# Optimization experiments

Hardware: AMD Instinct MI355X
Metric: run time of the kernel (lower is better)

Reference implementation:

```python
import jax, jax.numpy as jnp
import numpy as np

SHAPES = ((100, 100), (50, 50), (25, 25))  # (H_l, W_l) per level
D, HEADS, HD, L, P = 256, 8, 32, 3, 4


def setup_inputs() -> dict:
    key = jax.random.key(0)
    ks = jax.random.split(key, 12)
    B = 2
    Nq = sum(h * w for h, w in SHAPES)  # 13125
    inp = {
        "query": jax.random.normal(ks[0], (B, Nq, D), jnp.float32),
        "reference_points": jax.random.uniform(ks[1], (B, Nq, L, 2), jnp.float32),
        "value0": jax.random.normal(ks[2], (B, SHAPES[0][0] * SHAPES[0][1], D), jnp.float32),
        "value1": jax.random.normal(ks[3], (B, SHAPES[1][0] * SHAPES[1][1], D), jnp.float32),
        "value2": jax.random.normal(ks[4], (B, SHAPES[2][0] * SHAPES[2][1], D), jnp.float32),
        "W_val": jax.random.normal(ks[5], (D, D), jnp.float32) * 0.05,
        "b_val": jnp.zeros((D,), jnp.float32),
        "W_off": jax.random.normal(ks[6], (D, HEADS * L * P * 2), jnp.float32) * 0.01,
        "b_off": jax.random.normal(ks[7], (HEADS * L * P * 2,), jnp.float32) * 2.0,
        "W_attn": jax.random.normal(ks[8], (D, HEADS * L * P), jnp.float32) * 0.02,
        "b_attn": jnp.zeros((HEADS * L * P,), jnp.float32),
        "W_out": jax.random.normal(ks[9], (D, D), jnp.float32) * 0.05,
        "b_out": jnp.zeros((D,), jnp.float32),
    }
    return inp


def _bilinear_sample(v, Hl, Wl, loc):
    """v: (B, heads, Hl*Wl, hd); loc: (B, Nq, heads, P, 2) normalized coords in [0,1].
    Matches torch F.grid_sample(mode='bilinear', padding_mode='zeros', align_corners=False)
    applied to grid = 2*loc - 1. Returns (B, Nq, heads, P, hd)."""
    B, heads, _, hd = v.shape
    Nq, Pn = loc.shape[1], loc.shape[3]
    # align_corners=False: pixel = ((g+1)*size - 1)/2 with g = 2*loc-1  ->  loc*size - 0.5
    x = loc[..., 0] * Wl - 0.5
    y = loc[..., 1] * Hl - 0.5
    x0 = jnp.floor(x)
    y0 = jnp.floor(y)
    wx1 = x - x0
    wy1 = y - y0
    out = jnp.zeros((B, Nq, heads, Pn, hd), v.dtype)
    for xi, wx in ((x0, 1.0 - wx1), (x0 + 1.0, wx1)):
        for yi, wy in ((y0, 1.0 - wy1), (y0 + 1.0, wy1)):
            inb = (xi >= 0) & (xi < Wl) & (yi >= 0) & (yi < Hl)
            idx = (jnp.clip(yi, 0, Hl - 1) * Wl + jnp.clip(xi, 0, Wl - 1)).astype(jnp.int32)
            idx_t = idx.transpose(0, 2, 1, 3).reshape(B, heads, Nq * Pn)  # (B,H,Nq*P)
            g = jnp.take_along_axis(v, idx_t[..., None], axis=2)  # (B,H,Nq*P,hd)
            g = g.reshape(B, heads, Nq, Pn, hd).transpose(0, 2, 1, 3, 4)
            w = (wx * wy * inb).astype(v.dtype)  # (B,Nq,heads,P)
            out = out + g * w[..., None]
    return out


def _forward(query, reference_points, values, W_val, b_val, W_off, b_off, W_attn, b_attn, W_out, b_out):
    B, Nq, _ = query.shape
    offs = (query @ W_off + b_off).reshape(B, Nq, HEADS, L, P, 2)
    attn = jax.nn.softmax((query @ W_attn + b_attn).reshape(B, Nq, HEADS, L * P), axis=-1)
    attn = attn.reshape(B, Nq, HEADS, L, P)
    out = jnp.zeros((B, Nq, HEADS, HD), query.dtype)
    for lvl, (Hl, Wl) in enumerate(SHAPES):
        # project values, split heads: (B, heads, H*W, hd)
        v = (values[lvl] @ W_val + b_val).reshape(B, Hl * Wl, HEADS, HD).transpose(0, 2, 1, 3)
        norm = jnp.array([Wl, Hl], query.dtype)
        loc = reference_points[:, :, lvl][:, :, None, None, :] + offs[:, :, :, lvl] / norm  # (B,Nq,heads,P,2)
        sampled = _bilinear_sample(v, Hl, Wl, loc)  # (B,Nq,heads,P,hd)
        out = out + jnp.einsum('bnhp,bnhpd->bnhd', attn[:, :, :, lvl], sampled)
    out = out.reshape(B, Nq, D)
    return out @ W_out + b_out  # dropout is identity at eval


def reference(query, reference_points, value0, value1, value2, W_val, b_val, W_off, b_off, W_attn, b_attn, W_out, b_out):
    return _forward(query, reference_points, (value0, value1, value2), W_val, b_val, W_off, b_off, W_attn, b_attn, W_out, b_out)
```

## Files before the change

### kernel.cpp

```cpp
#include <hip/hip_runtime.h>
#include <hip/hip_bf16.h>
#include <math.h>

#define BATCH 2
#define NQ    13125
#define MQ    26250
#define DM    256
#define NH    8
#define HDIM  32
#define NL    3
#define NP    4
#define NTOK  13125
#define HSTRIDE (MQ * 32)

typedef __attribute__((ext_vector_type(8))) short bf16x8;
typedef __attribute__((ext_vector_type(4))) float f32x4;
typedef __attribute__((ext_vector_type(2))) float f32x2;

__device__ __forceinline__ short f2bf(float f) {
    unsigned u = __float_as_uint(f);
    unsigned r = (u + 0x7FFFu + ((u >> 16) & 1u)) >> 16;
    return (short)r;
}
__device__ __forceinline__ float bf2f(unsigned short u) {
    return __uint_as_float((unsigned)u << 16);
}
__device__ __forceinline__ unsigned cvt_pk_bf16(float lo, float hi) {
    unsigned r;
    asm("v_cvt_pk_bf16_f32 %0, %1, %2" : "=v"(r) : "v"(lo), "v"(hi));
    return r;
}

__device__ __forceinline__ void gld_lds16(const short* g, short* l) {
    __builtin_amdgcn_global_load_lds(
        (const __attribute__((address_space(1))) unsigned int*)g,
        (__attribute__((address_space(3))) unsigned int*)l, 16, 0, 0);
}

__global__ __launch_bounds__(256) void wprep_kernel(const float* __restrict__ Wv,
                                                    const float* __restrict__ Wo,
                                                    const float* __restrict__ Wa,
                                                    const float* __restrict__ Wu,
                                                    short* __restrict__ Wt)
{
    const int bid = blockIdx.x;
    const int w  = bid >> 8;
    const int Ns[5]   = {256, 192, 96, 256, 96};
    const int Offs[5] = {0, 65536, 114688, 163840, 139264};
    const int N = Ns[w];
    const int flat = (bid & 255) * 256 + threadIdx.x;
    const int n = flat >> 8, k = flat & 255;
    if (n >= N) return;
    if (w == 4) { Wt[139264 + n * 256 + k] = 0; return; }
    const float* W = (w == 0) ? Wv : ((w == 1) ? Wo : ((w == 2) ? Wa : Wu));
    Wt[Offs[w] + n * 256 + k] = f2bf(W[k * N + n]);
}

__global__ __launch_bounds__(512) void gemm5_kernel(const float* __restrict__ query,
                                                    const float* __restrict__ v0,
                                                    const float* __restrict__ v1,
                                                    const float* __restrict__ v2,
                                                    const short* __restrict__ Wt_val,
                                                    const short* __restrict__ Wt_off,
                                                    const float* __restrict__ b_val,
                                                    const float* __restrict__ b_off,
                                                    const float* __restrict__ b_attn,
                                                    short* __restrict__ vws,
                                                    float* __restrict__ offs,
                                                    float* __restrict__ lgts)
{
    const int e = (blockIdx.x & 7) * 129 + (blockIdx.x >> 3);
    if (e >= 1030) return;
    const int y  = e % 5;
    const int m0 = (e / 5) * 128;

    __shared__ short As[2][128 * 32];
    __shared__ short Bs[2][128 * 32];

    const int tid  = threadIdx.x;
    const bool isv = (y < 2);
    const short* Wt = isv ? Wt_val : Wt_off;
    const int n0 = isv ? y * 128 : (y - 2) * 128;

    const int r  = tid >> 2;
    const int qh = tid & 3;
    const int gm = m0 + r;
    const int gmc = (gm < MQ) ? gm : (MQ - 1);
    const float* Arow;
    if (isv) {
        const int b  = gmc / NTOK;
        const int rr = gmc % NTOK;
        if (rr < 10000)      Arow = v0 + (size_t)(b * 10000 + rr) * 256;
        else if (rr < 12500) Arow = v1 + (size_t)(b * 2500 + rr - 10000) * 256;
        else                 Arow = v2 + (size_t)(b * 625 + rr - 12500) * 256;
    } else {
        Arow = query + (size_t)gmc * 256;
    }
    const int pA = (qh ^ ((r >> 1) & 3)) << 3;

    const int kqs = qh ^ ((r >> 1) & 3);
    const short* gB = Wt + (size_t)(n0 + r) * 256 + kqs * 8;
    short* lB[2] = { Bs[0] + tid * 8, Bs[1] + tid * 8 };

    const int lane = tid & 63;
    const int wave = tid >> 6;
    const int wm   = (wave & 1) * 64;
    const int wn   = (wave >> 1) * 32;
    const int ml   = lane & 15;
    const int kq   = lane >> 4;

    f32x4 acc[4][2] = {};

    {
        gld_lds16(gB, lB[0]);
        const float4 a0 = *(const float4*)(Arow + qh * 8 + 0);
        const float4 a1 = *(const float4*)(Arow + qh * 8 + 4);
        union { bf16x8 v; unsigned u[4]; } t0;
        t0.u[0] = cvt_pk_bf16(a0.x, a0.y); t0.u[1] = cvt_pk_bf16(a0.z, a0.w);
        t0.u[2] = cvt_pk_bf16(a1.x, a1.y); t0.u[3] = cvt_pk_bf16(a1.z, a1.w);
        *(bf16x8*)(As[0] + r * 32 + pA) = t0.v;
    }
    __syncthreads();

#pragma unroll
    for (int t = 0; t < 8; ++t) {
        const int cur = t & 1, nxt = cur ^ 1;
        const int k0  = t * 32;

        float4 a0, a1;
        if (t < 7) {
            gld_lds16(gB + k0 + 32, lB[nxt]);
            a0 = *(const float4*)(Arow + k0 + 32 + qh * 8 + 0);
            a1 = *(const float4*)(Arow + k0 + 32 + qh * 8 + 4);
        }

        bf16x8 af[4], bfr[2];
#pragma unroll
        for (int ti = 0; ti < 4; ++ti) {
            const int rr = wm + ti * 16 + ml;
            af[ti] = *(const bf16x8*)&As[cur][rr * 32 + ((kq ^ ((rr >> 1) & 3)) << 3)];
        }
#pragma unroll
        for (int tj = 0; tj < 2; ++tj) {
            const int rr = wn + tj * 16 + ml;
            bfr[tj] = *(const bf16x8*)&Bs[cur][rr * 32 + ((kq ^ ((rr >> 1) & 3)) << 3)];
        }
#pragma unroll
        for (int ti = 0; ti < 4; ++ti)
#pragma unroll
            for (int tj = 0; tj < 2; ++tj)
                acc[ti][tj] = __builtin_amdgcn_mfma_f32_16x16x32_bf16(af[ti], bfr[tj], acc[ti][tj], 0, 0, 0);

        if (t < 7) {
            union { bf16x8 v; unsigned u[4]; } t0;
            t0.u[0] = cvt_pk_bf16(a0.x, a0.y); t0.u[1] = cvt_pk_bf16(a0.z, a0.w);
            t0.u[2] = cvt_pk_bf16(a1.x, a1.y); t0.u[3] = cvt_pk_bf16(a1.z, a1.w);
            *(bf16x8*)(As[nxt] + r * 32 + pA) = t0.v;
        }
        __syncthreads();
    }

#pragma unroll
    for (int tj = 0; tj < 2; ++tj) {
        const int gn = n0 + wn + tj * 16 + ml;
#pragma unroll
        for (int ti = 0; ti < 4; ++ti) {
#pragma unroll
            for (int rr = 0; rr < 4; ++rr) {
                const int gmo = m0 + wm + ti * 16 + kq * 4 + rr;
                if (gmo >= MQ) continue;
                const float v = acc[ti][tj][rr];
                if (isv) {
                    vws[(size_t)(gn >> 5) * HSTRIDE + (size_t)gmo * 32 + (gn & 31)] =
                        f2bf(v + b_val[gn]);
                } else {
                    if (gn < 192)      offs[(size_t)gmo * 192 + gn]        = v + b_off[gn];
                    else if (gn < 288) lgts[(size_t)gmo * 96 + (gn - 192)] = v + b_attn[gn - 192];
                }
            }
        }
    }
}

__global__ __launch_bounds__(512) void ogemm_kernel(const short* __restrict__ A,
                                                    const short* __restrict__ Wt,
                                                    const float* __restrict__ bias,
                                                    float* __restrict__ C)
{
    const int e = (blockIdx.x & 7) * 52 + (blockIdx.x >> 3);
    if (e >= 412) return;
    const int m0 = (e >> 1) * 128;
    const int n0 = (e & 1) * 128;

    __shared__ short As[2][128 * 32];
    __shared__ short Bs[2][128 * 32];

    const int tid  = threadIdx.x;
    const int r    = tid >> 2;
    const int kqs  = (tid & 3) ^ ((r >> 1) & 3);
    const short* gA = A  + (size_t)(m0 + r) * 256 + kqs * 8;
    const short* gB = Wt + (size_t)(n0 + r) * 256 + kqs * 8;
    short* lA[2] = { As[0] + tid * 8, As[1] + tid * 8 };
    short* lB[2] = { Bs[0] + tid * 8, Bs[1] + tid * 8 };
    const bool aok = (m0 + r) < MQ;

    const int lane = tid & 63;
    const int wave = tid >> 6;
    const int wm   = (wave & 1) * 64;
    const int wn   = (wave >> 1) * 32;
    const int ml   = lane & 15;
    const int kq   = lane >> 4;

    f32x4 acc[4][2] = {};

    if (aok) gld_lds16(gA, lA[0]);
    gld_lds16(gB, lB[0]);
    __syncthreads();

#pragma unroll
    for (int t = 0; t < 8; ++t) {
        const int cur = t & 1, nxt = cur ^ 1;
        const int k0  = t * 32;

        if (t < 7) {
            if (aok) gld_lds16(gA + k0 + 32, lA[nxt]);
            gld_lds16(gB + k0 + 32, lB[nxt]);
        }

        bf16x8 af[4], bfr[2];
#pragma unroll
        for (int ti = 0; ti < 4; ++ti) {
            const int rr = wm + ti * 16 + ml;
            af[ti] = *(const bf16x8*)&As[cur][rr * 32 + ((kq ^ ((rr >> 1) & 3)) << 3)];
        }
#pragma unroll
        for (int tj = 0; tj < 2; ++tj) {
            const int rr = wn + tj * 16 + ml;
            bfr[tj] = *(const bf16x8*)&Bs[cur][rr * 32 + ((kq ^ ((rr >> 1) & 3)) << 3)];
        }
#pragma unroll
        for (int ti = 0; ti < 4; ++ti)
#pragma unroll
            for (int tj = 0; tj < 2; ++tj)
                acc[ti][tj] = __builtin_amdgcn_mfma_f32_16x16x32_bf16(af[ti], bfr[tj], acc[ti][tj], 0, 0, 0);

        __syncthreads();
    }

#pragma unroll
    for (int tj = 0; tj < 2; ++tj) {
        const int gn = n0 + wn + tj * 16 + ml;
        const float bb = bias[gn];
#pragma unroll
        for (int ti = 0; ti < 4; ++ti) {
#pragma unroll
            for (int rr = 0; rr < 4; ++rr) {
                const int gm = m0 + wm + ti * 16 + kq * 4 + rr;
                if (gm >= MQ) continue;
                C[(size_t)gm * 256 + gn] = acc[ti][tj][rr] + bb;
            }
        }
    }
}

__device__ __forceinline__ void pk_acc(f32x2 (&acc)[4], uint4 u, float w) {
    f32x2 w2 = {w, w};
    unsigned ud[4] = {u.x, u.y, u.z, u.w};
#pragma unroll
    for (int d = 0; d < 4; ++d) {
        f32x2 v2;
        v2.x = __uint_as_float(ud[d] << 16);
        v2.y = __uint_as_float(ud[d] & 0xFFFF0000u);
        asm("v_pk_fma_f32 %0, %1, %2, %0" : "+v"(acc[d]) : "v"(v2), "v"(w2));
    }
}

__global__ __launch_bounds__(128) void sample_kernel(const short* __restrict__ vws,
                                                     const float* __restrict__ offs,
                                                     const float* __restrict__ logits,
                                                     const float* __restrict__ refp,
                                                     short* __restrict__ mid)
{
    const int bid = blockIdx.x;
    const int h   = bid & 7;
    const int q0  = (bid >> 3) * 32;
    if (q0 >= MQ) return;
    const int tid = threadIdx.x;

    __shared__ float  s_lg[32][13];
    __shared__ float  s_ref[32][6];
    __shared__ float2 s_stat[32];
    __shared__ float4 s_w[32][13];
    __shared__ int4   s_i[32][13];

    for (int idx = tid; idx < 384; idx += 128) {
        const int qq = idx / 12, i = idx % 12;
        const int q = q0 + qq;
        if (q < MQ) s_lg[qq][i] = logits[(size_t)q * 96 + h * 12 + i];
    }
    for (int idx = tid; idx < 192; idx += 128) {
        const int qq = idx / 6, j = idx % 6;
        const int q = q0 + qq;
        if (q < MQ) s_ref[qq][j] = refp[(size_t)q * 6 + j];
    }
    __syncthreads();

    if (tid < 32) {
        const int qq = tid;
        if (q0 + qq < MQ) {
            float mx = -1e30f;
#pragma unroll
            for (int i = 0; i < 12; ++i) mx = fmaxf(mx, s_lg[qq][i]);
            float ssum = 0.f;
#pragma unroll
            for (int i = 0; i < 12; ++i) ssum += __expf(s_lg[qq][i] - mx);
            s_stat[qq].x = mx;
            s_stat[qq].y = 1.f / ssum;
        }
    }
    __syncthreads();

    for (int idx = tid; idx < 384; idx += 128) {
        const int qq = idx / 12, i = idx % 12;
        const int q  = q0 + qq;
        if (q >= MQ) continue;
        const int b  = q / NQ;
        const int l  = i >> 2, p = i & 3;

        const int Hs[3] = {100, 50, 25};
        const int Wz[3] = {100, 50, 25};
        const int Lo[3] = {0, 10000, 12500};
        const int Wl = Wz[l], Hl = Hs[l];
        const float fW = (float)Wl, fH = (float)Hl;

        const float aw = __expf(s_lg[qq][i] - s_stat[qq].x) * s_stat[qq].y;

        const int oi = h * 24 + l * 8 + p * 2;
        const float2 offp = *(const float2*)(offs + (size_t)q * 192 + oi);
        const float rx = s_ref[qq][l * 2 + 0];
        const float ry = s_ref[qq][l * 2 + 1];

        const float x = (rx + offp.x / fW) * fW - 0.5f;
        const float y = (ry + offp.y / fH) * fH - 0.5f;
        const float x0f = floorf(x), y0f = floorf(y);
        const int   x0 = (int)x0f,  y0 = (int)y0f;
        const float wx1 = x - x0f, wy1 = y - y0f;
        const float wx0 = 1.f - wx1, wy0 = 1.f - wy1;

        const bool xin0 = (x0 >= 0) && (x0 < Wl);
        const bool xin1 = (x0 + 1 >= 0) && (x0 + 1 < Wl);
        const bool yin0 = (y0 >= 0) && (y0 < Hl);
        const bool yin1 = (y0 + 1 >= 0) && (y0 + 1 < Hl);

        const int cx0 = min(max(x0, 0), Wl - 1);
        const int cx1 = min(max(x0 + 1, 0), Wl - 1);
        const int cy0 = min(max(y0, 0), Hl - 1);
        const int cy1 = min(max(y0 + 1, 0), Hl - 1);

        const int base = b * NTOK + Lo[l];
        int4 idxv;
        idxv.x = (base + cy0 * Wl + cx0) << 5;
        idxv.y = (base + cy0 * Wl + cx1) << 5;
        idxv.z = (base + cy1 * Wl + cx0) << 5;
        idxv.w = (base + cy1 * Wl + cx1) << 5;

        float4 w;
        w.x = (xin0 && yin0) ? aw * wx0 * wy0 : 0.f;
        w.y = (xin1 && yin0) ? aw * wx1 * wy0 : 0.f;
        w.z = (xin0 && yin1) ? aw * wx0 * wy1 : 0.f;
        w.w = (xin1 && yin1) ? aw * wx1 * wy1 : 0.f;

        s_w[qq][i] = w;
        s_i[qq][i] = idxv;
    }
    __syncthreads();

    {
        const int qq = tid >> 2;
        const int q  = q0 + qq;
        if (q < MQ) {
            const int c8 = (tid & 3) * 8;
            const short* base = vws + (size_t)h * HSTRIDE + c8;

            float4 w_ = s_w[qq][0];
            int4  id_ = s_i[qq][0];
            uint4 a_ = *(const uint4*)(base + id_.x);
            uint4 b_ = *(const uint4*)(base + id_.y);
            uint4 c_ = *(const uint4*)(base + id_.z);
            uint4 d_ = *(const uint4*)(base + id_.w);

            f32x2 acc[4] = {};
#pragma unroll
            for (int s = 0; s < 12; ++s) {
                const float4 w = w_;
                const uint4 ua = a_, ub = b_, uc = c_, ud = d_;
                if (s < 11) {
                    w_  = s_w[qq][s + 1];
                    id_ = s_i[qq][s + 1];
                    a_ = *(const uint4*)(base + id_.x);
                    b_ = *(const uint4*)(base + id_.y);
                    c_ = *(const uint4*)(base + id_.z);
                    d_ = *(const uint4*)(base + id_.w);
                }
                pk_acc(acc, ua, w.x);
                pk_acc(acc, ub, w.y);
                pk_acc(acc, uc, w.z);
                pk_acc(acc, ud, w.w);
            }
            uint4 o;
            o.x = cvt_pk_bf16(acc[0].x, acc[0].y);
            o.y = cvt_pk_bf16(acc[1].x, acc[1].y);
            o.z = cvt_pk_bf16(acc[2].x, acc[2].y);
            o.w = cvt_pk_bf16(acc[3].x, acc[3].y);
            *(uint4*)(mid + (size_t)q * DM + h * HDIM + c8) = o;
        }
    }
}

extern "C" void kernel_launch(void* const* d_in, const int* in_sizes, int n_in,
                              void* d_out, int out_size, void* d_ws, size_t ws_size,
                              hipStream_t stream)
{
    const float* query  = (const float*)d_in[0];
    const float* refp   = (const float*)d_in[1];
    const float* v0     = (const float*)d_in[2];
    const float* v1     = (const float*)d_in[3];
    const float* v2     = (const float*)d_in[4];
    const float* W_val  = (const float*)d_in[5];
    const float* b_val  = (const float*)d_in[6];
    const float* W_off  = (const float*)d_in[7];
    const float* b_off  = (const float*)d_in[8];
    const float* W_attn = (const float*)d_in[9];
    const float* b_attn = (const float*)d_in[10];
    const float* W_out  = (const float*)d_in[11];
    const float* b_out  = (const float*)d_in[12];
    float* out = (float*)d_out;

    float* ws   = (float*)d_ws;
    float* offs = ws;
    float* lgts = offs + (size_t)MQ * 192;
    short* vws  = (short*)(lgts + (size_t)MQ * 96);
    short* mid  = vws + (size_t)MQ * DM;
    short* Wt   = mid + (size_t)MQ * DM;
    short* Wt_val = Wt;
    short* Wt_off = Wt + 65536;
    short* Wt_out = Wt + 163840;

    wprep_kernel<<<1280, 256, 0, stream>>>(W_val, W_off, W_attn, W_out, Wt);
    gemm5_kernel<<<1032, 512, 0, stream>>>(query, v0, v1, v2, Wt_val, Wt_off,
                                           b_val, b_off, b_attn, vws, offs, lgts);
    sample_kernel<<<6568, 128, 0, stream>>>(vws, offs, lgts, refp, mid);
    ogemm_kernel<<<416, 512, 0, stream>>>(mid, Wt_out, b_out, out);
}
```

Measured before the change: 200.7 us.

## Triple-buffer GEMM LDS tiles with explicit partial waitcnt barriers

Both the projection GEMM and the output GEMM move from double to triple buffering of the B (and, in the output GEMM, A) LDS tiles. Loads are issued two k-steps ahead, and `__syncthreads` is replaced by explicit s_waitcnt plus s_barrier, using vmcnt(2) so the newest loads stay in flight across the barrier. The out-of-range A-row guard in the output GEMM becomes a clamped row index, so all lanes issue loads uniformly. This aims to hide global-to-LDS latency better, at the cost of more LDS per block, which may reduce occupancy. Correctness depends on the hand-counted vmcnt values, and the projection GEMM's barrier waits only on lgkmcnt, not vmcnt, before reading the global_load_lds B tile.

After: 199.9 us, median of 2. No clear change (-0.4%).

```diff
diff --git a/kernel.cpp b/kernel.cpp
--- a/kernel.cpp
+++ b/kernel.cpp
@@ -35,6 +35,13 @@
     __builtin_amdgcn_global_load_lds(
         (const __attribute__((address_space(1))) unsigned int*)g,
         (__attribute__((address_space(3))) unsigned int*)l, 16, 0, 0);
+}
+
+__device__ __forceinline__ void fence_barrier_lgkm() {
+    asm volatile("s_waitcnt lgkmcnt(0)" ::: "memory");
+    __builtin_amdgcn_sched_barrier(0);
+    __builtin_amdgcn_s_barrier();
+    __builtin_amdgcn_sched_barrier(0);
 }
 
 __global__ __launch_bounds__(256) void wprep_kernel(const float* __restrict__ Wv,
@@ -75,7 +82,7 @@
     const int m0 = (e / 5) * 128;
 
     __shared__ short As[2][128 * 32];
-    __shared__ short Bs[2][128 * 32];
+    __shared__ short Bs[3][128 * 32];
 
     const int tid  = threadIdx.x;
     const bool isv = (y < 2);
@@ -100,7 +107,6 @@
 
     const int kqs = qh ^ ((r >> 1) & 3);
     const short* gB = Wt + (size_t)(n0 + r) * 256 + kqs * 8;
-    short* lB[2] = { Bs[0] + tid * 8, Bs[1] + tid * 8 };
 
     const int lane = tid & 63;
     const int wave = tid >> 6;
@@ -109,41 +115,46 @@
     const int ml   = lane & 15;
     const int kq   = lane >> 4;
 
+    float4 s0a, s0b, s1a, s1b;
+#define LOAD_SET0(T) { s0a = *(const float4*)(Arow + (T)*32 + qh*8 + 0); \
+                       s0b = *(const float4*)(Arow + (T)*32 + qh*8 + 4); }
+#define LOAD_SET1(T) { s1a = *(const float4*)(Arow + (T)*32 + qh*8 + 0); \
+                       s1b = *(const float4*)(Arow + (T)*32 + qh*8 + 4); }
+#define CVT_WRITE0(DST) { union { bf16x8 v; unsigned u[4]; } t0;          \
+        t0.u[0] = cvt_pk_bf16(s0a.x, s0a.y); t0.u[1] = cvt_pk_bf16(s0a.z, s0a.w); \
+        t0.u[2] = cvt_pk_bf16(s0b.x, s0b.y); t0.u[3] = cvt_pk_bf16(s0b.z, s0b.w); \
+        *(bf16x8*)((DST) + r * 32 + pA) = t0.v; }
+#define CVT_WRITE1(DST) { union { bf16x8 v; unsigned u[4]; } t0;          \
+        t0.u[0] = cvt_pk_bf16(s1a.x, s1a.y); t0.u[1] = cvt_pk_bf16(s1a.z, s1a.w); \
+        t0.u[2] = cvt_pk_bf16(s1b.x, s1b.y); t0.u[3] = cvt_pk_bf16(s1b.z, s1b.w); \
+        *(bf16x8*)((DST) + r * 32 + pA) = t0.v; }
+
     f32x4 acc[4][2] = {};
 
-    {
-        gld_lds16(gB, lB[0]);
-        const float4 a0 = *(const float4*)(Arow + qh * 8 + 0);
-        const float4 a1 = *(const float4*)(Arow + qh * 8 + 4);
-        union { bf16x8 v; unsigned u[4]; } t0;
-        t0.u[0] = cvt_pk_bf16(a0.x, a0.y); t0.u[1] = cvt_pk_bf16(a0.z, a0.w);
-        t0.u[2] = cvt_pk_bf16(a1.x, a1.y); t0.u[3] = cvt_pk_bf16(a1.z, a1.w);
-        *(bf16x8*)(As[0] + r * 32 + pA) = t0.v;
-    }
-    __syncthreads();
+    gld_lds16(gB + 0,  Bs[0] + tid * 8);
+    LOAD_SET0(0);
+    gld_lds16(gB + 32, Bs[1] + tid * 8);
+    LOAD_SET1(1);
+    CVT_WRITE0(As[0]);
+    fence_barrier_lgkm();
 
 #pragma unroll
     for (int t = 0; t < 8; ++t) {
-        const int cur = t & 1, nxt = cur ^ 1;
-        const int k0  = t * 32;
-
-        float4 a0, a1;
-        if (t < 7) {
-            gld_lds16(gB + k0 + 32, lB[nxt]);
-            a0 = *(const float4*)(Arow + k0 + 32 + qh * 8 + 0);
-            a1 = *(const float4*)(Arow + k0 + 32 + qh * 8 + 4);
+        if (t <= 5) {
+            gld_lds16(gB + (t + 2) * 32, Bs[(t + 2) % 3] + tid * 8);
+            if ((t & 1) == 0) LOAD_SET0(t + 2) else LOAD_SET1(t + 2)
         }
 
         bf16x8 af[4], bfr[2];
 #pragma unroll
         for (int ti = 0; ti < 4; ++ti) {
             const int rr = wm + ti * 16 + ml;
-            af[ti] = *(const bf16x8*)&As[cur][rr * 32 + ((kq ^ ((rr >> 1) & 3)) << 3)];
+            af[ti] = *(const bf16x8*)&As[t & 1][rr * 32 + ((kq ^ ((rr >> 1) & 3)) << 3)];
         }
 #pragma unroll
         for (int tj = 0; tj < 2; ++tj) {
             const int rr = wn + tj * 16 + ml;
-            bfr[tj] = *(const bf16x8*)&Bs[cur][rr * 32 + ((kq ^ ((rr >> 1) & 3)) << 3)];
+            bfr[tj] = *(const bf16x8*)&Bs[t % 3][rr * 32 + ((kq ^ ((rr >> 1) & 3)) << 3)];
         }
 #pragma unroll
         for (int ti = 0; ti < 4; ++ti)
@@ -152,13 +163,15 @@
                 acc[ti][tj] = __builtin_amdgcn_mfma_f32_16x16x32_bf16(af[ti], bfr[tj], acc[ti][tj], 0, 0, 0);
 
         if (t < 7) {
-            union { bf16x8 v; unsigned u[4]; } t0;
-            t0.u[0] = cvt_pk_bf16(a0.x, a0.y); t0.u[1] = cvt_pk_bf16(a0.z, a0.w);
-            t0.u[2] = cvt_pk_bf16(a1.x, a1.y); t0.u[3] = cvt_pk_bf16(a1.z, a1.w);
-            *(bf16x8*)(As[nxt] + r * 32 + pA) = t0.v;
-        }
-        __syncthreads();
-    }
+            if (((t + 1) & 1) == 0) CVT_WRITE0(As[(t + 1) & 1]) else CVT_WRITE1(As[(t + 1) & 1])
+        }
+
+        fence_barrier_lgkm();
+    }
+#undef LOAD_SET0
+#undef LOAD_SET1
+#undef CVT_WRITE0
+#undef CVT_WRITE1
 
 #pragma unroll
     for (int tj = 0; tj < 2; ++tj) {
@@ -192,17 +205,16 @@
     const int m0 = (e >> 1) * 128;
     const int n0 = (e & 1) * 128;
 
-    __shared__ short As[2][128 * 32];
-    __shared__ short Bs[2][128 * 32];
+    __shared__ short As[3][128 * 32];
+    __shared__ short Bs[3][128 * 32];
 
     const int tid  = threadIdx.x;
     const int r    = tid >> 2;
     const int kqs  = (tid & 3) ^ ((r >> 1) & 3);
-    const short* gA = A  + (size_t)(m0 + r) * 256 + kqs * 8;
+    const int gmr  = m0 + r;
+    const int gmrc = (gmr < MQ) ? gmr : (MQ - 1);
+    const short* gA = A  + (size_t)gmrc * 256 + kqs * 8;
     const short* gB = Wt + (size_t)(n0 + r) * 256 + kqs * 8;
-    short* lA[2] = { As[0] + tid * 8, As[1] + tid * 8 };
-    short* lB[2] = { Bs[0] + tid * 8, Bs[1] + tid * 8 };
-    const bool aok = (m0 + r) < MQ;
 
     const int lane = tid & 63;
     const int wave = tid >> 6;
@@ -213,30 +225,32 @@
 
     f32x4 acc[4][2] = {};
 
-    if (aok) gld_lds16(gA, lA[0]);
-    gld_lds16(gB, lB[0]);
-    __syncthreads();
+    gld_lds16(gA + 0,  As[0] + tid * 8);
+    gld_lds16(gB + 0,  Bs[0] + tid * 8);
+    gld_lds16(gA + 32, As[1] + tid * 8);
+    gld_lds16(gB + 32, Bs[1] + tid * 8);
+    asm volatile("s_waitcnt vmcnt(2)" ::: "memory");
+    __builtin_amdgcn_sched_barrier(0);
+    __builtin_amdgcn_s_barrier();
+    __builtin_amdgcn_sched_barrier(0);
 
 #pragma unroll
     for (int t = 0; t < 8; ++t) {
-        const int cur = t & 1, nxt = cur ^ 1;
-        const int k0  = t * 32;
-
-        if (t < 7) {
-            if (aok) gld_lds16(gA + k0 + 32, lA[nxt]);
-            gld_lds16(gB + k0 + 32, lB[nxt]);
+        if (t <= 5) {
+            gld_lds16(gA + (t + 2) * 32, As[(t + 2) % 3] + tid * 8);
+            gld_lds16(gB + (t + 2) * 32, Bs[(t + 2) % 3] + tid * 8);
         }
 
         bf16x8 af[4], bfr[2];
 #pragma unroll
         for (int ti = 0; ti < 4; ++ti) {
             const int rr = wm + ti * 16 + ml;
-            af[ti] = *(const bf16x8*)&As[cur][rr * 32 + ((kq ^ ((rr >> 1) & 3)) << 3)];
+            af[ti] = *(const bf16x8*)&As[t % 3][rr * 32 + ((kq ^ ((rr >> 1) & 3)) << 3)];
         }
 #pragma unroll
         for (int tj = 0; tj < 2; ++tj) {
             const int rr = wn + tj * 16 + ml;
-            bfr[tj] = *(const bf16x8*)&Bs[cur][rr * 32 + ((kq ^ ((rr >> 1) & 3)) << 3)];
+            bfr[tj] = *(const bf16x8*)&Bs[t % 3][rr * 32 + ((kq ^ ((rr >> 1) & 3)) << 3)];
         }
 #pragma unroll
         for (int ti = 0; ti < 4; ++ti)
@@ -244,7 +258,13 @@
             for (int tj = 0; tj < 2; ++tj)
                 acc[ti][tj] = __builtin_amdgcn_mfma_f32_16x16x32_bf16(af[ti], bfr[tj], acc[ti][tj], 0, 0, 0);
 
-        __syncthreads();
+        if (t < 7) {
+            if (t <= 5) asm volatile("s_waitcnt vmcnt(2)" ::: "memory");
+            else        asm volatile("s_waitcnt vmcnt(0)" ::: "memory");
+            __builtin_amdgcn_sched_barrier(0);
+            __builtin_amdgcn_s_barrier();
+            __builtin_amdgcn_sched_barrier(0);
+        }
     }
 
 #pragma unroll
```

## Load GEMM fragments directly from global memory into registers, bypassing LDS

Applied to the files above, without the earlier changes.

Both projection GEMM kernels stop staging A and B tiles in shared memory. Each lane now loads its MFMA fragments straight from global memory into double-buffered registers, and the block-wide barriers are removed. This cuts LDS traffic and synchronisation, but each block loses the data reuse LDS gave it: a row is now fetched separately by every wave that needs it, so global and L2 traffic rise. Register pressure also grows, which may lower occupancy.

After: 277.7 us. 38.4% more time.

```diff
diff --git a/kernel.cpp b/kernel.cpp
--- a/kernel.cpp
+++ b/kernel.cpp
@@ -29,12 +29,6 @@
     unsigned r;
     asm("v_cvt_pk_bf16_f32 %0, %1, %2" : "=v"(r) : "v"(lo), "v"(hi));
     return r;
-}
-
-__device__ __forceinline__ void gld_lds16(const short* g, short* l) {
-    __builtin_amdgcn_global_load_lds(
-        (const __attribute__((address_space(1))) unsigned int*)g,
-        (__attribute__((address_space(3))) unsigned int*)l, 16, 0, 0);
 }
 
 __global__ __launch_bounds__(256) void wprep_kernel(const float* __restrict__ Wv,
@@ -74,33 +68,10 @@
     const int y  = e % 5;
     const int m0 = (e / 5) * 128;
 
-    __shared__ short As[2][128 * 32];
-    __shared__ short Bs[2][128 * 32];
-
     const int tid  = threadIdx.x;
     const bool isv = (y < 2);
     const short* Wt = isv ? Wt_val : Wt_off;
     const int n0 = isv ? y * 128 : (y - 2) * 128;
-
-    const int r  = tid >> 2;
-    const int qh = tid & 3;
-    const int gm = m0 + r;
-    const int gmc = (gm < MQ) ? gm : (MQ - 1);
-    const float* Arow;
-    if (isv) {
-        const int b  = gmc / NTOK;
-        const int rr = gmc % NTOK;
-        if (rr < 10000)      Arow = v0 + (size_t)(b * 10000 + rr) * 256;
-        else if (rr < 12500) Arow = v1 + (size_t)(b * 2500 + rr - 10000) * 256;
-        else                 Arow = v2 + (size_t)(b * 625 + rr - 12500) * 256;
-    } else {
-        Arow = query + (size_t)gmc * 256;
-    }
-    const int pA = (qh ^ ((r >> 1) & 3)) << 3;
-
-    const int kqs = qh ^ ((r >> 1) & 3);
-    const short* gB = Wt + (size_t)(n0 + r) * 256 + kqs * 8;
-    short* lB[2] = { Bs[0] + tid * 8, Bs[1] + tid * 8 };
 
     const int lane = tid & 63;
     const int wave = tid >> 6;
@@ -109,56 +80,64 @@
     const int ml   = lane & 15;
     const int kq   = lane >> 4;
 
+    const float* Ar[4];
+#pragma unroll
+    for (int ti = 0; ti < 4; ++ti) {
+        int gm = m0 + wm + ti * 16 + ml;
+        if (gm >= MQ) gm = MQ - 1;
+        const float* p;
+        if (isv) {
+            const int b  = gm / NTOK;
+            const int rr = gm % NTOK;
+            if (rr < 10000)      p = v0 + (size_t)(b * 10000 + rr) * 256;
+            else if (rr < 12500) p = v1 + (size_t)(b * 2500 + rr - 10000) * 256;
+            else                 p = v2 + (size_t)(b * 625 + rr - 12500) * 256;
+        } else {
+            p = query + (size_t)gm * 256;
+        }
+        Ar[ti] = p + kq * 8;
+    }
+    const short* Br[2];
+#pragma unroll
+    for (int tj = 0; tj < 2; ++tj)
+        Br[tj] = Wt + (size_t)(n0 + wn + tj * 16 + ml) * 256 + kq * 8;
+
     f32x4 acc[4][2] = {};
-
-    {
-        gld_lds16(gB, lB[0]);
-        const float4 a0 = *(const float4*)(Arow + qh * 8 + 0);
-        const float4 a1 = *(const float4*)(Arow + qh * 8 + 4);
-        union { bf16x8 v; unsigned u[4]; } t0;
-        t0.u[0] = cvt_pk_bf16(a0.x, a0.y); t0.u[1] = cvt_pk_bf16(a0.z, a0.w);
-        t0.u[2] = cvt_pk_bf16(a1.x, a1.y); t0.u[3] = cvt_pk_bf16(a1.z, a1.w);
-        *(bf16x8*)(As[0] + r * 32 + pA) = t0.v;
-    }
-    __syncthreads();
+    float4 a0[2][4], a1[2][4];
+    bf16x8 bfr[2][2];
+
+#define LOADS(SET, T) {                                               \
+    _Pragma("unroll") for (int ti = 0; ti < 4; ++ti) {                \
+        a0[SET][ti] = *(const float4*)(Ar[ti] + (T) * 32);            \
+        a1[SET][ti] = *(const float4*)(Ar[ti] + (T) * 32 + 4);        \
+    }                                                                 \
+    _Pragma("unroll") for (int tj = 0; tj < 2; ++tj)                  \
+        bfr[SET][tj] = *(const bf16x8*)(Br[tj] + (T) * 32); }
+
+    LOADS(0, 0)
 
 #pragma unroll
     for (int t = 0; t < 8; ++t) {
-        const int cur = t & 1, nxt = cur ^ 1;
-        const int k0  = t * 32;
-
-        float4 a0, a1;
-        if (t < 7) {
-            gld_lds16(gB + k0 + 32, lB[nxt]);
-            a0 = *(const float4*)(Arow + k0 + 32 + qh * 8 + 0);
-            a1 = *(const float4*)(Arow + k0 + 32 + qh * 8 + 4);
-        }
-
-        bf16x8 af[4], bfr[2];
+        const int cur = t & 1;
+        if (t < 7) LOADS(cur ^ 1, t + 1)
+
+        bf16x8 af[4];
 #pragma unroll
         for (int ti = 0; ti < 4; ++ti) {
-            const int rr = wm + ti * 16 + ml;
-            af[ti] = *(const bf16x8*)&As[cur][rr * 32 + ((kq ^ ((rr >> 1) & 3)) << 3)];
-        }
-#pragma unroll
-        for (int tj = 0; tj < 2; ++tj) {
-            const int rr = wn + tj * 16 + ml;
-            bfr[tj] = *(const bf16x8*)&Bs[cur][rr * 32 + ((kq ^ ((rr >> 1) & 3)) << 3)];
+            union { bf16x8 v; unsigned u[4]; } tmp;
+            tmp.u[0] = cvt_pk_bf16(a0[cur][ti].x, a0[cur][ti].y);
+            tmp.u[1] = cvt_pk_bf16(a0[cur][ti].z, a0[cur][ti].w);
+            tmp.u[2] = cvt_pk_bf16(a1[cur][ti].x, a1[cur][ti].y);
+            tmp.u[3] = cvt_pk_bf16(a1[cur][ti].z, a1[cur][ti].w);
+            af[ti] = tmp.v;
         }
 #pragma unroll
         for (int ti = 0; ti < 4; ++ti)
 #pragma unroll
             for (int tj = 0; tj < 2; ++tj)
-                acc[ti][tj] = __builtin_amdgcn_mfma_f32_16x16x32_bf16(af[ti], bfr[tj], acc[ti][tj], 0, 0, 0);
-
-        if (t < 7) {
-            union { bf16x8 v; unsigned u[4]; } t0;
-            t0.u[0] = cvt_pk_bf16(a0.x, a0.y); t0.u[1] = cvt_pk_bf16(a0.z, a0.w);
-            t0.u[2] = cvt_pk_bf16(a1.x, a1.y); t0.u[3] = cvt_pk_bf16(a1.z, a1.w);
-            *(bf16x8*)(As[nxt] + r * 32 + pA) = t0.v;
-        }
-        __syncthreads();
-    }
+                acc[ti][tj] = __builtin_amdgcn_mfma_f32_16x16x32_bf16(af[ti], bfr[cur][tj], acc[ti][tj], 0, 0, 0);
+    }
+#undef LOADS
 
 #pragma unroll
     for (int tj = 0; tj < 2; ++tj) {
@@ -192,18 +171,7 @@
     const int m0 = (e >> 1) * 128;
     const int n0 = (e & 1) * 128;
 
-    __shared__ short As[2][128 * 32];
-    __shared__ short Bs[2][128 * 32];
-
     const int tid  = threadIdx.x;
-    const int r    = tid >> 2;
-    const int kqs  = (tid & 3) ^ ((r >> 1) & 3);
-    const short* gA = A  + (size_t)(m0 + r) * 256 + kqs * 8;
-    const short* gB = Wt + (size_t)(n0 + r) * 256 + kqs * 8;
-    short* lA[2] = { As[0] + tid * 8, As[1] + tid * 8 };
-    short* lB[2] = { Bs[0] + tid * 8, Bs[1] + tid * 8 };
-    const bool aok = (m0 + r) < MQ;
-
     const int lane = tid & 63;
     const int wave = tid >> 6;
     const int wm   = (wave & 1) * 64;
@@ -211,41 +179,40 @@
     const int ml   = lane & 15;
     const int kq   = lane >> 4;
 
+    const short* Ar[4];
+#pragma unroll
+    for (int ti = 0; ti < 4; ++ti) {
+        int gm = m0 + wm + ti * 16 + ml;
+        if (gm >= MQ) gm = MQ - 1;
+        Ar[ti] = A + (size_t)gm * 256 + kq * 8;
+    }
+    const short* Br[2];
+#pragma unroll
+    for (int tj = 0; tj < 2; ++tj)
+        Br[tj] = Wt + (size_t)(n0 + wn + tj * 16 + ml) * 256 + kq * 8;
+
     f32x4 acc[4][2] = {};
-
-    if (aok) gld_lds16(gA, lA[0]);
-    gld_lds16(gB, lB[0]);
-    __syncthreads();
+    bf16x8 afr[2][4], bfr[2][2];
+
+#define LOADS(SET, T) {                                               \
+    _Pragma("unroll") for (int ti = 0; ti < 4; ++ti)                  \
+        afr[SET][ti] = *(const bf16x8*)(Ar[ti] + (T) * 32);           \
+    _Pragma("unroll") for (int tj = 0; tj < 2; ++tj)                  \
+        bfr[SET][tj] = *(const bf16x8*)(Br[tj] + (T) * 32); }
+
+    LOADS(0, 0)
 
 #pragma unroll
     for (int t = 0; t < 8; ++t) {
-        const int cur = t & 1, nxt = cur ^ 1;
-        const int k0  = t * 32;
-
-        if (t < 7) {
-            if (aok) gld_lds16(gA + k0 + 32, lA[nxt]);
-            gld_lds16(gB + k0 + 32, lB[nxt]);
-        }
-
-        bf16x8 af[4], bfr[2];
-#pragma unroll
-        for (int ti = 0; ti < 4; ++ti) {
-            const int rr = wm + ti * 16 + ml;
-            af[ti] = *(const bf16x8*)&As[cur][rr * 32 + ((kq ^ ((rr >> 1) & 3)) << 3)];
-        }
-#pragma unroll
-        for (int tj = 0; tj < 2; ++tj) {
-            const int rr = wn + tj * 16 + ml;
-            bfr[tj] = *(const bf16x8*)&Bs[cur][rr * 32 + ((kq ^ ((rr >> 1) & 3)) << 3)];
-        }
+        const int cur = t & 1;
+        if (t < 7) LOADS(cur ^ 1, t + 1)
 #pragma unroll
         for (int ti = 0; ti < 4; ++ti)
 #pragma unroll
             for (int tj = 0; tj < 2; ++tj)
-                acc[ti][tj] = __builtin_amdgcn_mfma_f32_16x16x32_bf16(af[ti], bfr[tj], acc[ti][tj], 0, 0, 0);
-
-        __syncthreads();
-    }
+                acc[ti][tj] = __builtin_amdgcn_mfma_f32_16x16x32_bf16(afr[cur][ti], bfr[cur][tj], acc[ti][tj], 0, 0, 0);
+    }
+#undef LOADS
 
 #pragma unroll
     for (int tj = 0; tj < 2; ++tj) {
```
